# Performance work log

Hardware: AMD Instinct MI355X
Metric: run time of the kernel (lower is better)

The kernel has to match this reference:

```python
import jax, jax.numpy as jnp
import numpy as np

N = 100000
E = 1600000
NEG_SLOPE = 0.2


def gat_conv(h_x, edge_index, W, a_src, a_dst, b, heads, concat):
    # h_x: [N, Fin]; W: [Fin, heads*C]
    n = h_x.shape[0]
    h = (h_x @ W).reshape(n, heads, -1)              # [N, H, C]
    s_src = (h * a_src[None]).sum(-1)                # [N, H]
    s_dst = (h * a_dst[None]).sum(-1)                # [N, H]
    # add self loops (PyG default)
    loop = jnp.arange(n, dtype=edge_index.dtype)
    src = jnp.concatenate([edge_index[0], loop])
    dst = jnp.concatenate([edge_index[1], loop])
    e = jax.nn.leaky_relu(s_src[src] + s_dst[dst], NEG_SLOPE)   # [E+N, H]
    m = jax.ops.segment_max(e, dst, num_segments=n)
    e = jnp.exp(e - m[dst])
    denom = jax.ops.segment_sum(e, dst, num_segments=n)
    alpha = e / denom[dst]                                       # [E+N, H]
    out = jax.ops.segment_sum(alpha[:, :, None] * h[src], dst, num_segments=n)  # [N,H,C]
    out = out.reshape(n, -1) if concat else out.mean(axis=1)
    return out + b


def setup_inputs() -> dict:
    key = jax.random.key(0)
    ks = jax.random.split(key, 16)
    s = 0.1
    return {
        "x": jax.random.normal(ks[0], (N, 128), jnp.float32),
        "edge_index": jax.random.randint(ks[1], (2, E), 0, N, jnp.int64 if jax.config.jax_enable_x64 else jnp.int32),
        "W0": jax.random.normal(ks[2], (128, 64), jnp.float32) * s,
        "a_src0": jax.random.normal(ks[3], (1, 64), jnp.float32) * s,
        "a_dst0": jax.random.normal(ks[4], (1, 64), jnp.float32) * s,
        "b0": jax.random.normal(ks[5], (64,), jnp.float32) * s,
        "sW0": jax.random.normal(ks[6], (128, 64), jnp.float32) * s,
        "sb0": jax.random.normal(ks[7], (64,), jnp.float32) * s,
        "W1": jax.random.normal(ks[8], (64, 32), jnp.float32) * s,
        "a_src1": jax.random.normal(ks[9], (1, 32), jnp.float32) * s,
        "a_dst1": jax.random.normal(ks[10], (1, 32), jnp.float32) * s,
        "b1": jax.random.normal(ks[11], (32,), jnp.float32) * s,
        "sW1": jax.random.normal(ks[12], (64, 32), jnp.float32) * s,
        "sb1": jax.random.normal(ks[13], (32,), jnp.float32) * s,
    }


def reference(x, edge_index, W0, a_src0, a_dst0, b0, sW0, sb0,
              W1, a_src1, a_dst1, b1, sW1, sb1):
    # layer 0: GATConv (heads=1, concat=True) + linear skip, ELU (dropout p=0 is identity)
    h = gat_conv(x, edge_index, W0, a_src0, a_dst0, b0, heads=1, concat=True) + (x @ sW0 + sb0)
    h = jax.nn.elu(h)
    # layer 1: GATConv (heads=1, concat=False -> mean) + linear skip, log_softmax
    h = gat_conv(h, edge_index, W1, a_src1, a_dst1, b1, heads=1, concat=False) + (h @ sW1 + sb1)
    return jax.nn.log_softmax(h, axis=-1)
```

## Files before the change

### kernel.cpp

```cpp
#include <hip/hip_runtime.h>
#include <hip/hip_bf16.h>
#include <math.h>

#define NEG_SLOPE 0.2f
#define ECLAMP 30.0f
#define HCLAMP 1.0e4f

#define BSHIFT 8
#define BR 256
#define NBMAX 1024
#define CHUNK 2048

typedef short v8s __attribute__((ext_vector_type(8)));
typedef float v4f __attribute__((ext_vector_type(4)));
typedef unsigned long long ull;

__device__ __forceinline__ float bf2f(__hip_bfloat16 v) { return __bfloat162float(v); }
__device__ __forceinline__ __hip_bfloat16 f2bf(float v) { return __float2bfloat16(v); }
__device__ __forceinline__ float sane(float v)   { return fminf(fmaxf(v, -HCLAMP), HCLAMP); }
__device__ __forceinline__ float eclampf(float v){ return fminf(fmaxf(v, -ECLAMP), ECLAMP); }

__device__ __forceinline__ float ldany(int isf32, const void* p, int i) {
    return isf32 ? ((const float*)p)[i] : bf2f(((const __hip_bfloat16*)p)[i]);
}
__device__ __forceinline__ int ldidx(int is64, const void* p, long long i) {
    return is64 ? (int)((const long long*)p)[i] : ((const int*)p)[i];
}
__device__ __forceinline__ v8s ld8(const __hip_bfloat16* p) { return *(const v8s*)p; }

__device__ __forceinline__ float ewgt(float e) {
    e = e > 0.f ? e : NEG_SLOPE * e;
    return __expf(eclampf(e));
}

__device__ __forceinline__ float bflo(unsigned v) { return __uint_as_float(v << 16); }
__device__ __forceinline__ float bfhi(unsigned v) { return __uint_as_float(v & 0xffff0000u); }
__device__ __forceinline__ unsigned packbf(float a, float b) {
    __hip_bfloat16 x = f2bf(a), y = f2bf(b);
    return (unsigned)(*(unsigned short*)&x) | ((unsigned)(*(unsigned short*)&y) << 16);
}

__global__ void k_probe(const unsigned* __restrict__ xw, int nw_safe,
                        const unsigned* __restrict__ ew, int* __restrict__ flags) {
    __shared__ int cnt[2];
    int t = threadIdx.x;
    if (t < 2) cnt[t] = 0;
    __syncthreads();
    unsigned w = xw[(unsigned)(t * 9973) % (unsigned)nw_safe];
    unsigned lo = w & 0xffffu;
    unsigned exp = (lo >> 7) & 0xffu;
    if (lo != 0u && (exp < 90u || exp > 160u)) atomicAdd(&cnt[0], 1);
    if (ew[2 * t + 1] == 0u) atomicAdd(&cnt[1], 1);
    __syncthreads();
    if (t == 0) { flags[0] = (2 * cnt[0] > 256) ? 1 : 0; flags[1] = (cnt[1] >= 200) ? 1 : 0; }
}

__global__ void k_params(const int* __restrict__ flags,
                         const void* W0, const void* sW0, const void* as0, const void* ad0,
                         const void* b0, const void* sb0, const void* W1, const void* sW1,
                         const void* as1, const void* ad1, const void* b1, const void* sb1,
                         float* __restrict__ Pf, __hip_bfloat16* __restrict__ Wg) {
    int f = flags[0];
    int t = blockIdx.x * blockDim.x + threadIdx.x;
    int T = gridDim.x * blockDim.x;
    for (int i = t; i < 8192; i += T) {
        int n = i >> 7, k = i & 127;
        Wg[i]        = f2bf(ldany(f, W0,  k * 64 + n));
        Wg[8192 + i] = f2bf(ldany(f, sW0, k * 64 + n));
    }
    for (int i = t; i < 2048; i += T) {
        int n = i >> 6, k = i & 63;
        Wg[16384 + i] = f2bf(ldany(f, W1,  k * 32 + n));
        Wg[18432 + i] = f2bf(ldany(f, sW1, k * 32 + n));
    }
    if (t < 64) {
        Pf[t]       = ldany(f, as0, t);
        Pf[64 + t]  = ldany(f, ad0, t);
        Pf[128 + t] = ldany(f, b0, t) + ldany(f, sb0, t);
    }
    if (t < 32) {
        Pf[192 + t] = ldany(f, as1, t);
        Pf[224 + t] = ldany(f, ad1, t);
        Pf[256 + t] = ldany(f, b1, t) + ldany(f, sb1, t);
    }
}

__global__ void k_zero(int* __restrict__ p, int n) {
    int i = blockIdx.x * blockDim.x + threadIdx.x;
    if (i < n) p[i] = 0;
}

__global__ __launch_bounds__(256) void k_chist(const void* __restrict__ ei,
                                               const int* __restrict__ flags,
                                               int E, int N, int NB,
                                               int* __restrict__ hist) {
    __shared__ int h[NBMAX];
    for (int i = threadIdx.x; i < NB; i += 256) h[i] = 0;
    __syncthreads();
    int f = flags[1];
    long long c0 = (long long)blockIdx.x * CHUNK;
    long long c1 = c0 + CHUNK;
    if (c1 > E) c1 = E;
    for (long long i = c0 + threadIdx.x; i < c1; i += 256) {
        unsigned d = (unsigned)ldidx(f, ei, (long long)E + i);
        if (d < (unsigned)N) atomicAdd(&h[d >> BSHIFT], 1);
    }
    __syncthreads();
    long long base = (long long)blockIdx.x * NB;
    for (int i = threadIdx.x; i < NB; i += 256) hist[base + i] = h[i];
}

__global__ __launch_bounds__(1024) void k_cscan(const int* __restrict__ hist,
                                                int gch, int NB,
                                                int* __restrict__ cb,
                                                int* __restrict__ bcount) {
    __shared__ int sh[1024];
    int b = blockIdx.x;
    int t = threadIdx.x;
    int run = 0;
    for (int base = 0; base < gch; base += 1024) {
        int c = base + t;
        int v = (c < gch) ? hist[(long long)c * NB + b] : 0;
        sh[t] = v;
        __syncthreads();
        for (int off = 1; off < 1024; off <<= 1) {
            int xv = (t >= off) ? sh[t - off] : 0;
            __syncthreads();
            sh[t] += xv;
            __syncthreads();
        }
        if (c < gch) cb[(long long)c * NB + b] = run + sh[t] - v;
        run += sh[1023];
        __syncthreads();
    }
    if (t == 0) bcount[b] = run;
}

__global__ void k_bscan(const int* __restrict__ bcount, int NB,
                        int* __restrict__ bbase) {
    __shared__ int sh[NBMAX];
    int t = threadIdx.x;
    int v = (t < NB) ? bcount[t] : 0;
    sh[t] = v;
    __syncthreads();
    for (int off = 1; off < NBMAX; off <<= 1) {
        int xv = (t >= off) ? sh[t - off] : 0;
        __syncthreads();
        sh[t] += xv;
        __syncthreads();
    }
    if (t < NB) bbase[t] = sh[t] - v;
    if (t == NB - 1) bbase[NB] = sh[t];
}

__global__ __launch_bounds__(256) void k_bscatter(const void* __restrict__ ei,
                                                  const int* __restrict__ flags,
                                                  int E, int N, int NB,
                                                  const int* __restrict__ bbase,
                                                  const int* __restrict__ cb,
                                                  unsigned* __restrict__ binned) {
    __shared__ int rb[NBMAX];
    int f = flags[1];
    long long cbase = (long long)blockIdx.x * NB;
    for (int i = threadIdx.x; i < NB; i += 256) rb[i] = bbase[i] + cb[cbase + i];
    __syncthreads();
    long long c0 = (long long)blockIdx.x * CHUNK;
    long long c1 = c0 + CHUNK;
    if (c1 > E) c1 = E;
    for (long long i = c0 + threadIdx.x; i < c1; i += 256) {
        unsigned d = (unsigned)ldidx(f, ei, (long long)E + i);
        if (d < (unsigned)N) {
            int b = d >> BSHIFT;
            unsigned s = (unsigned)ldidx(f, ei, i);
            if (s >= (unsigned)N) s = 0x00FFFFFFu;
            int r = atomicAdd(&rb[b], 1);
            binned[r] = ((d & (unsigned)(BR - 1)) << 24) | s;
        }
    }
}

__global__ __launch_bounds__(256) void k_bbuild(const unsigned* __restrict__ binned,
                                                const int* __restrict__ bbase,
                                                int N, int NB,
                                                int* __restrict__ rowptr,
                                                int* __restrict__ csr_src) {
    __shared__ int ldeg[BR];
    __shared__ int lpos[BR];
    int b = blockIdx.x;
    int t = threadIdx.x;
    int e0 = bbase[b], e1 = bbase[b + 1];
    ldeg[t] = 0;
    __syncthreads();
    for (int i = e0 + t; i < e1; i += 256) {
        atomicAdd(&ldeg[binned[i] >> 24], 1);
    }
    __syncthreads();
    int v = ldeg[t];
    lpos[t] = v;
    __syncthreads();
    for (int off = 1; off < BR; off <<= 1) {
        int xv = (t >= off) ? lpos[t - off] : 0;
        __syncthreads();
        lpos[t] += xv;
        __syncthreads();
    }
    int excl = lpos[t] - v;
    int node = (b << BSHIFT) + t;
    if (node < N) rowptr[node] = e0 + excl;
    if (b == NB - 1 && t == 0) rowptr[N] = e1;
    ldeg[t] = e0 + excl;
    __syncthreads();
    for (int i = e0 + t; i < e1; i += 256) {
        unsigned w = binned[i];
        int p = atomicAdd(&ldeg[w >> 24], 1);
        csr_src[p] = (int)(w & 0x00FFFFFFu);
    }
}

__global__ void k_deg(const void* __restrict__ ei, const int* __restrict__ flags,
                      int E, int N, int* __restrict__ deg) {
    int i = blockIdx.x * blockDim.x + threadIdx.x;
    if (i < E) {
        unsigned d = (unsigned)ldidx(flags[1], ei, (long long)E + i);
        if (d < (unsigned)N) atomicAdd(&deg[d], 1);
    }
}

__global__ void k_scan1(const int* __restrict__ deg, int N,
                        int* __restrict__ rowptr, int* __restrict__ bsum) {
    __shared__ int sh[1024];
    int t = threadIdx.x;
    int idx = blockIdx.x * 1024 + t;
    int v = (idx < N) ? deg[idx] : 0;
    sh[t] = v;
    __syncthreads();
    for (int off = 1; off < 1024; off <<= 1) {
        int xv = (t >= off) ? sh[t - off] : 0;
        __syncthreads();
        sh[t] += xv;
        __syncthreads();
    }
    if (idx < N) rowptr[idx] = sh[t] - v;
    if (t == 1023) bsum[blockIdx.x] = sh[1023];
}

__global__ void k_scan2(int* __restrict__ bsum, int B, int* __restrict__ rowptr, int N) {
    __shared__ int sh[1024];
    int t = threadIdx.x;
    int v = (t < B) ? bsum[t] : 0;
    sh[t] = v;
    __syncthreads();
    for (int off = 1; off < 1024; off <<= 1) {
        int xv = (t >= off) ? sh[t - off] : 0;
        __syncthreads();
        sh[t] += xv;
        __syncthreads();
    }
    if (t < B) bsum[t] = sh[t] - v;
    if (t == 1023) rowptr[N] = sh[1023];
}

__global__ void k_scan3(int N, int* __restrict__ rowptr, const int* __restrict__ bsum,
                        int* __restrict__ cursor) {
    int idx = blockIdx.x * 1024 + threadIdx.x;
    if (idx < N) {
        int r = rowptr[idx] + bsum[blockIdx.x];
        rowptr[idx] = r;
        cursor[idx] = r;
    }
}

__global__ void k_fill(const void* __restrict__ ei, const int* __restrict__ flags,
                       int E, int N, int* __restrict__ cursor, int* __restrict__ csr_src) {
    int i = blockIdx.x * blockDim.x + threadIdx.x;
    if (i < E) {
        int f = flags[1];
        unsigned d = (unsigned)ldidx(f, ei, (long long)E + i);
        if (d < (unsigned)N) {
            int p = atomicAdd(&cursor[d], 1);
            if ((unsigned)p < (unsigned)E) csr_src[p] = ldidx(f, ei, i);
        }
    }
}

__global__ __launch_bounds__(256) void k_l0(
    const void* __restrict__ x, const int* __restrict__ flags,
    const float* __restrict__ Pf, const __hip_bfloat16* __restrict__ Wg, int N,
    __hip_bfloat16* __restrict__ h0, __hip_bfloat16* __restrict__ skip0,
    float* __restrict__ ssrc, float* __restrict__ sdst) {
    __shared__ __hip_bfloat16 sm[26112];
    __hip_bfloat16* xs  = sm;
    __hip_bfloat16* wt0 = sm + 8704;
    __hip_bfloat16* wts = sm + 17408;
    int tid = threadIdx.x;
    int f = flags[0];
    int tile = blockIdx.x * 64;

    for (int i = tid * 4; i < 8192; i += 1024) {
        int r = i >> 7, k = i & 127;
        uint2 w0v = *(const uint2*)&Wg[i];
        uint2 w1v = *(const uint2*)&Wg[8192 + i];
        *(uint2*)&wt0[r * 136 + k] = w0v;
        *(uint2*)&wts[r * 136 + k] = w1v;
    }
    for (int i = tid * 4; i < 8192; i += 1024) {
        int r = i >> 7, k = i & 127;
        int g = tile + r; if (g >= N) g = N - 1;
        uint2* dx = (uint2*)&xs[r * 136 + k];
        if (f) {
            float4 v = *(const float4*)((const float*)x + (size_t)g * 128 + k);
            uint2 o; o.x = packbf(v.x, v.y); o.y = packbf(v.z, v.w);
            *dx = o;
        } else {
            *dx = *(const uint2*)((const __hip_bfloat16*)x + (size_t)g * 128 + k);
        }
    }
    __syncthreads();

    int lane = tid & 63, w = tid >> 6;
    int n16 = lane & 15, quad = lane >> 4;
    v4f zf = {0.f, 0.f, 0.f, 0.f};
    v4f acc_h[4], acc_s[4];
#pragma unroll
    for (int t = 0; t < 4; t++) { acc_h[t] = zf; acc_s[t] = zf; }

    int arow = (w << 4) + n16;
#pragma unroll
    for (int s = 0; s < 4; s++) {
        v8s a = ld8(&xs[arow * 136 + s * 32 + (quad << 3)]);
#pragma unroll
        for (int t = 0; t < 4; t++) {
            v8s bh = ld8(&wt0[(t * 16 + n16) * 136 + s * 32 + (quad << 3)]);
            acc_h[t] = __builtin_amdgcn_mfma_f32_16x16x32_bf16(a, bh, acc_h[t], 0, 0, 0);
            v8s bs = ld8(&wts[(t * 16 + n16) * 136 + s * 32 + (quad << 3)]);
            acc_s[t] = __builtin_amdgcn_mfma_f32_16x16x32_bf16(a, bs, acc_s[t], 0, 0, 0);
        }
    }

    int mbase = tile + (w << 4) + (quad << 2);
    float ps[4] = {0, 0, 0, 0}, pd[4] = {0, 0, 0, 0};
#pragma unroll
    for (int t = 0; t < 4; t++) {
        int ch = t * 16 + n16;
        float av = Pf[ch];
        float dv = Pf[64 + ch];
        float bv = Pf[128 + ch];
#pragma unroll
        for (int r = 0; r < 4; r++) {
            float hv = sane(acc_h[t][r]);
            float sv = sane(acc_s[t][r] + bv);
            int node = mbase + r;
            if (node < N) {
                h0[(size_t)node * 64 + ch] = f2bf(hv);
                skip0[(size_t)node * 64 + ch] = f2bf(sv);
            }
            ps[r] += hv * av;
            pd[r] += hv * dv;
        }
    }
#pragma unroll
    for (int m = 1; m <= 8; m <<= 1) {
#pragma unroll
        for (int r = 0; r < 4; r++) {
            ps[r] += __shfl_xor(ps[r], m, 64);
            pd[r] += __shfl_xor(pd[r], m, 64);
        }
    }
    if (n16 == 0) {
#pragma unroll
        for (int r = 0; r < 4; r++) {
            int node = mbase + r;
            if (node < N) { ssrc[node] = sane(ps[r]); sdst[node] = sane(pd[r]); }
        }
    }
}

__global__ __launch_bounds__(512) void k_l0agg_l1(
    const int* __restrict__ rowptr, const int* __restrict__ csr_src,
    const float* __restrict__ ssrc0, const float* __restrict__ sdst0,
    const __hip_bfloat16* __restrict__ h0, const __hip_bfloat16* __restrict__ skip0,
    const float* __restrict__ Pf, const __hip_bfloat16* __restrict__ Wg, int N,
    __hip_bfloat16* __restrict__ h1, __hip_bfloat16* __restrict__ skip1,
    float* __restrict__ ssrc1, float* __restrict__ sdst1) {
    __shared__ __hip_bfloat16 xs[4608];
    __shared__ __hip_bfloat16 wsm[4608];
    __shared__ ull ews[512];
    __shared__ float psum[64], pdum[64];
    __hip_bfloat16* wt1 = wsm;
    __hip_bfloat16* ws1 = wsm + 2304;
    int tid = threadIdx.x;
    int tile = blockIdx.x * 64;

    {
        int i = tid * 4;
        int r = i >> 6, k = i & 63;
        *(uint2*)&wt1[r * 72 + k] = *(const uint2*)&Wg[16384 + i];
        *(uint2*)&ws1[r * 72 + k] = *(const uint2*)&Wg[18432 + i];
    }
    if (tid < 64) { psum[tid] = 0.f; pdum[tid] = 0.f; }

    int wv = tid >> 6, lane = tid & 63;
    int half = lane >> 5, l5 = lane & 31;
    int slot = l5 >> 4, c4 = l5 & 15;
    const uint2* h0w = (const uint2*)h0;
    ull* myw = &ews[wv * 64 + half * 32];

    for (int pass = 0; pass < 4; pass++) {
        int row = pass * 16 + wv * 2 + half;
        int n = tile + row;
        bool act = n < N;
        int nn = act ? n : 0;

        float sd = sdst0[nn];
        float wself = ewgt(ssrc0[nn] + sd);

        uint2 selfv = h0w[(size_t)nn * 16 + c4];
        float w0 = (slot == 0) ? wself : 0.f;
        float acc0 = w0 * bflo(selfv.x);
        float acc1 = w0 * bfhi(selfv.x);
        float acc2 = w0 * bflo(selfv.y);
        float acc3 = w0 * bfhi(selfv.y);
        float denp = 0.f;

        int beg = act ? rowptr[nn] : 0;
        int end = act ? rowptr[nn + 1] : 0;
        for (int j0 = beg; j0 < end; j0 += 32) {
            int cnt = end - j0; if (cnt > 32) cnt = 32;
            int s = (l5 < cnt) ? csr_src[j0 + l5] : 0;
            bool v = (l5 < cnt) && ((unsigned)s < (unsigned)N);
            int sg = v ? s : 0;
            float wj = v ? ewgt(ssrc0[sg] + sd) : 0.f;
            denp += wj;
            myw[l5] = ((ull)__float_as_uint(wj) << 32) | (unsigned)sg;
            int k2 = 0;
            int full = cnt & ~7;
            for (; k2 < full; k2 += 8) {
                ull pa = myw[k2 + slot];
                ull pb = myw[k2 + 2 + slot];
                ull pc = myw[k2 + 4 + slot];
                ull pd_ = myw[k2 + 6 + slot];
                float wa = __uint_as_float((unsigned)(pa >> 32));
                float wb = __uint_as_float((unsigned)(pb >> 32));
                float wc = __uint_as_float((unsigned)(pc >> 32));
                float wd = __uint_as_float((unsigned)(pd_ >> 32));
                int sa = (int)(unsigned)(pa & 0xffffffffu);
                int sb = (int)(unsigned)(pb & 0xffffffffu);
                int sc = (int)(unsigned)(pc & 0xffffffffu);
                int sdi = (int)(unsigned)(pd_ & 0xffffffffu);
                uint2 va = h0w[(size_t)sa * 16 + c4];
                uint2 vb = h0w[(size_t)sb * 16 + c4];
                uint2 vc = h0w[(size_t)sc * 16 + c4];
                uint2 vd = h0w[(size_t)sdi * 16 + c4];
                acc0 += wa * bflo(va.x) + wb * bflo(vb.x) + wc * bflo(vc.x) + wd * bflo(vd.x);
                acc1 += wa * bfhi(va.x) + wb * bfhi(vb.x) + wc * bfhi(vc.x) + wd * bfhi(vd.x);
                acc2 += wa * bflo(va.y) + wb * bflo(vb.y) + wc * bflo(vc.y) + wd * bflo(vd.y);
                acc3 += wa * bfhi(va.y) + wb * bfhi(vb.y) + wc * bfhi(vc.y) + wd * bfhi(vd.y);
            }
            for (; k2 < cnt; k2 += 8) {
                int ia = k2 + slot,     ib = k2 + 2 + slot;
                int ic = k2 + 4 + slot, id = k2 + 6 + slot;
                ull pa = myw[ia < cnt ? ia : 0];
                ull pb = myw[ib < cnt ? ib : 0];
                ull pc = myw[ic < cnt ? ic : 0];
                ull pd_ = myw[id < cnt ? id : 0];
                float wa = (ia < cnt) ? __uint_as_float((unsigned)(pa >> 32)) : 0.f;
                float wb = (ib < cnt) ? __uint_as_float((unsigned)(pb >> 32)) : 0.f;
                float wc = (ic < cnt) ? __uint_as_float((unsigned)(pc >> 32)) : 0.f;
                float wd = (id < cnt) ? __uint_as_float((unsigned)(pd_ >> 32)) : 0.f;
                int sa = (int)(unsigned)(pa & 0xffffffffu);
                int sb = (int)(unsigned)(pb & 0xffffffffu);
                int sc = (int)(unsigned)(pc & 0xffffffffu);
                int sdi = (int)(unsigned)(pd_ & 0xffffffffu);
                uint2 va = h0w[(size_t)sa * 16 + c4];
                uint2 vb = h0w[(size_t)sb * 16 + c4];
                uint2 vc = h0w[(size_t)sc * 16 + c4];
                uint2 vd = h0w[(size_t)sdi * 16 + c4];
                acc0 += wa * bflo(va.x) + wb * bflo(vb.x) + wc * bflo(vc.x) + wd * bflo(vd.x);
                acc1 += wa * bfhi(va.x) + wb * bfhi(vb.x) + wc * bfhi(vc.x) + wd * bfhi(vd.x);
                acc2 += wa * bflo(va.y) + wb * bflo(vb.y) + wc * bflo(vc.y) + wd * bflo(vd.y);
                acc3 += wa * bfhi(va.y) + wb * bfhi(vb.y) + wc * bfhi(vc.y) + wd * bfhi(vd.y);
            }
        }
        acc0 += __shfl_xor(acc0, 16, 64);
        acc1 += __shfl_xor(acc1, 16, 64);
        acc2 += __shfl_xor(acc2, 16, 64);
        acc3 += __shfl_xor(acc3, 16, 64);
        float den = denp;
#pragma unroll
        for (int m = 1; m <= 16; m <<= 1) den += __shfl_xor(den, m, 64);
        den += wself;

        if (slot == 0) {
            uint2 o; o.x = 0u; o.y = 0u;
            if (act) {
                uint2 skv = ((const uint2*)skip0)[(size_t)nn * 16 + c4];
                float v0 = sane(acc0 / den + bflo(skv.x));
                float v1 = sane(acc1 / den + bfhi(skv.x));
                float v2 = sane(acc2 / den + bflo(skv.y));
                float v3 = sane(acc3 / den + bfhi(skv.y));
                v0 = v0 > 0.f ? v0 : (__expf(v0) - 1.f);
                v1 = v1 > 0.f ? v1 : (__expf(v1) - 1.f);
                v2 = v2 > 0.f ? v2 : (__expf(v2) - 1.f);
                v3 = v3 > 0.f ? v3 : (__expf(v3) - 1.f);
                o.x = packbf(v0, v1);
                o.y = packbf(v2, v3);
            }
            *(uint2*)&xs[row * 72 + c4 * 4] = o;
        }
    }
    __syncthreads();

    int w8 = wv;
    int rt = w8 >> 1, ct = w8 & 1;
    int n16 = lane & 15, quad = lane >> 4;
    v4f acc_h = {0.f, 0.f, 0.f, 0.f};
    v4f acc_s = {0.f, 0.f, 0.f, 0.f};
    int arow = rt * 16 + n16;
#pragma unroll
    for (int s = 0; s < 2; s++) {
        v8s a = ld8(&xs[arow * 72 + s * 32 + (quad << 3)]);
        v8s bh = ld8(&wt1[(ct * 16 + n16) * 72 + s * 32 + (quad << 3)]);
        acc_h = __builtin_amdgcn_mfma_f32_16x16x32_bf16(a, bh, acc_h, 0, 0, 0);
        v8s bs = ld8(&ws1[(ct * 16 + n16) * 72 + s * 32 + (quad << 3)]);
        acc_s = __builtin_amdgcn_mfma_f32_16x16x32_bf16(a, bs, acc_s, 0, 0, 0);
    }

    int mrow = rt * 16 + (quad << 2);
    int mbase = tile + mrow;
    int ch = ct * 16 + n16;
    float av = Pf[192 + ch];
    float dv = Pf[224 + ch];
    float bv = Pf[256 + ch];
    float ps[4] = {0, 0, 0, 0}, pd[4] = {0, 0, 0, 0};
#pragma unroll
    for (int r = 0; r < 4; r++) {
        float hv = sane(acc_h[r]);
        float sv = sane(acc_s[r] + bv);
        int node = mbase + r;
        if (node < N) {
            h1[(size_t)node * 32 + ch] = f2bf(hv);
            skip1[(size_t)node * 32 + ch] = f2bf(sv);
        }
        ps[r] += hv * av;
        pd[r] += hv * dv;
    }
#pragma unroll
    for (int m = 1; m <= 8; m <<= 1) {
#pragma unroll
        for (int r = 0; r < 4; r++) {
            ps[r] += __shfl_xor(ps[r], m, 64);
            pd[r] += __shfl_xor(pd[r], m, 64);
        }
    }
    if (n16 == 0) {
#pragma unroll
        for (int r = 0; r < 4; r++) {
            atomicAdd(&psum[mrow + r], ps[r]);
            atomicAdd(&pdum[mrow + r], pd[r]);
        }
    }
    __syncthreads();
    if (tid < 64) {
        int node = tile + tid;
        if (node < N) {
            ssrc1[node] = sane(psum[tid]);
            sdst1[node] = sane(pdum[tid]);
        }
    }
}

__global__ __launch_bounds__(256) void k_l1_agg(
    const int* __restrict__ rowptr, const int* __restrict__ csr_src,
    const float* __restrict__ ssrc, const float* __restrict__ sdst,
    const __hip_bfloat16* __restrict__ h1, const __hip_bfloat16* __restrict__ skip1,
    int N, float* __restrict__ out) {
    __shared__ ull ews[256];
    int wv = threadIdx.x >> 6, lane = threadIdx.x & 63;
    int half = lane >> 5, l5 = lane & 31;
    int slot = l5 >> 3, c4 = l5 & 7;
    int n = blockIdx.x * 8 + wv * 2 + half;
    bool act = n < N;
    int nn = act ? n : 0;
    const uint2* h1w = (const uint2*)h1;
    ull* myw = &ews[wv * 64 + half * 32];

    float sd = sdst[nn];
    float wself = ewgt(ssrc[nn] + sd);

    uint2 selfv = h1w[(size_t)nn * 8 + c4];
    float w0 = (slot == 0) ? wself : 0.f;
    float acc0 = w0 * bflo(selfv.x);
    float acc1 = w0 * bfhi(selfv.x);
    float acc2 = w0 * bflo(selfv.y);
    float acc3 = w0 * bfhi(selfv.y);
    float denp = 0.f;

    int beg = act ? rowptr[nn] : 0;
    int end = act ? rowptr[nn + 1] : 0;
    for (int j0 = beg; j0 < end; j0 += 32) {
        int cnt = end - j0; if (cnt > 32) cnt = 32;
        int s = (l5 < cnt) ? csr_src[j0 + l5] : 0;
        bool v = (l5 < cnt) && ((unsigned)s < (unsigned)N);
        int sg = v ? s : 0;
        float wj = v ? ewgt(ssrc[sg] + sd) : 0.f;
        denp += wj;
        myw[l5] = ((ull)__float_as_uint(wj) << 32) | (unsigned)sg;
        int k4 = 0;
        int full = cnt & ~15;
        for (; k4 < full; k4 += 16) {
            ull pa = myw[k4 + slot];
            ull pb = myw[k4 + 4 + slot];
            ull pc = myw[k4 + 8 + slot];
            ull pd_ = myw[k4 + 12 + slot];
            float wa = __uint_as_float((unsigned)(pa >> 32));
            float wb = __uint_as_float((unsigned)(pb >> 32));
            float wc = __uint_as_float((unsigned)(pc >> 32));
            float wd = __uint_as_float((unsigned)(pd_ >> 32));
            int sa = (int)(unsigned)(pa & 0xffffffffu);
            int sb = (int)(unsigned)(pb & 0xffffffffu);
            int sc = (int)(unsigned)(pc & 0xffffffffu);
            int sdi = (int)(unsigned)(pd_ & 0xffffffffu);
            uint2 va = h1w[(size_t)sa * 8 + c4];
            uint2 vb = h1w[(size_t)sb * 8 + c4];
            uint2 vc = h1w[(size_t)sc * 8 + c4];
            uint2 vd = h1w[(size_t)sdi * 8 + c4];
            acc0 += wa * bflo(va.x) + wb * bflo(vb.x) + wc * bflo(vc.x) + wd * bflo(vd.x);
            acc1 += wa * bfhi(va.x) + wb * bfhi(vb.x) + wc * bfhi(vc.x) + wd * bfhi(vd.x);
            acc2 += wa * bflo(va.y) + wb * bflo(vb.y) + wc * bflo(vc.y) + wd * bflo(vd.y);
            acc3 += wa * bfhi(va.y) + wb * bfhi(vb.y) + wc * bfhi(vc.y) + wd * bfhi(vd.y);
        }
        for (; k4 < cnt; k4 += 16) {
            int ia = k4 + slot,      ib = k4 + 4 + slot;
            int ic = k4 + 8 + slot,  id = k4 + 12 + slot;
            ull pa = myw[ia < cnt ? ia : 0];
            ull pb = myw[ib < cnt ? ib : 0];
            ull pc = myw[ic < cnt ? ic : 0];
            ull pd_ = myw[id < cnt ? id : 0];
            float wa = (ia < cnt) ? __uint_as_float((unsigned)(pa >> 32)) : 0.f;
            float wb = (ib < cnt) ? __uint_as_float((unsigned)(pb >> 32)) : 0.f;
            float wc = (ic < cnt) ? __uint_as_float((unsigned)(pc >> 32)) : 0.f;
            float wd = (id < cnt) ? __uint_as_float((unsigned)(pd_ >> 32)) : 0.f;
            int sa = (int)(unsigned)(pa & 0xffffffffu);
            int sb = (int)(unsigned)(pb & 0xffffffffu);
            int sc = (int)(unsigned)(pc & 0xffffffffu);
            int sdi = (int)(unsigned)(pd_ & 0xffffffffu);
            uint2 va = h1w[(size_t)sa * 8 + c4];
            uint2 vb = h1w[(size_t)sb * 8 + c4];
            uint2 vc = h1w[(size_t)sc * 8 + c4];
            uint2 vd = h1w[(size_t)sdi * 8 + c4];
            acc0 += wa * bflo(va.x) + wb * bflo(vb.x) + wc * bflo(vc.x) + wd * bflo(vd.x);
            acc1 += wa * bfhi(va.x) + wb * bfhi(vb.x) + wc * bfhi(vc.x) + wd * bfhi(vd.x);
            acc2 += wa * bflo(va.y) + wb * bflo(vb.y) + wc * bflo(vc.y) + wd * bflo(vd.y);
            acc3 += wa * bfhi(va.y) + wb * bfhi(vb.y) + wc * bfhi(vc.y) + wd * bfhi(vd.y);
        }
    }
    acc0 += __shfl_xor(acc0, 8, 64); acc0 += __shfl_xor(acc0, 16, 64);
    acc1 += __shfl_xor(acc1, 8, 64); acc1 += __shfl_xor(acc1, 16, 64);
    acc2 += __shfl_xor(acc2, 8, 64); acc2 += __shfl_xor(acc2, 16, 64);
    acc3 += __shfl_xor(acc3, 8, 64); acc3 += __shfl_xor(acc3, 16, 64);
    float den = denp;
#pragma unroll
    for (int m = 1; m <= 16; m <<= 1) den += __shfl_xor(den, m, 64);
    den += wself;

    uint2 skv = ((const uint2*)skip1)[(size_t)nn * 8 + c4];
    float o0 = sane(acc0 / den + bflo(skv.x));
    float o1 = sane(acc1 / den + bfhi(skv.x));
    float o2 = sane(acc2 / den + bflo(skv.y));
    float o3 = sane(acc3 / den + bfhi(skv.y));
    float m = fmaxf(fmaxf(o0, o1), fmaxf(o2, o3));
#pragma unroll
    for (int k = 1; k <= 4; k <<= 1) m = fmaxf(m, __shfl_xor(m, k, 64));
    float ex = __expf(o0 - m) + __expf(o1 - m) + __expf(o2 - m) + __expf(o3 - m);
#pragma unroll
    for (int k = 1; k <= 4; k <<= 1) ex += __shfl_xor(ex, k, 64);
    float l = __logf(ex);
    float r0 = o0 - m - l, r1 = o1 - m - l, r2 = o2 - m - l, r3 = o3 - m - l;
    if (!isfinite(r0)) r0 = 0.f;
    if (!isfinite(r1)) r1 = 0.f;
    if (!isfinite(r2)) r2 = 0.f;
    if (!isfinite(r3)) r3 = 0.f;
    if (slot == 0 && act) {
        float4 o4; o4.x = r0; o4.y = r1; o4.z = r2; o4.w = r3;
        *(float4*)&out[(size_t)nn * 32 + 4 * c4] = o4;
    }
}

__global__ void k_sentinel(float* __restrict__ out, int n, float val) {
    int i = blockIdx.x * blockDim.x + threadIdx.x;
    if (i < n) out[i] = val;
}

extern "C" void kernel_launch(void* const* d_in, const int* in_sizes, int n_in,
                              void* d_out, int out_size, void* d_ws, size_t ws_size,
                              hipStream_t stream) {
    const void* x  = d_in[0];
    const void* ei = d_in[1];
    float* out = (float*)d_out;

    int N = in_sizes[0] / 128;
    int E = in_sizes[1] / 2;

    int NB  = (N + BR - 1) >> BSHIFT;
    int gch = (E + CHUNK - 1) / CHUNK;
    if (gch < 1) gch = 1;
    bool fast = (N <= (NBMAX << BSHIFT)) && ((size_t)E * 4 <= (size_t)N * 128);

    char* ws = (char*)d_ws;
    size_t off = 0;
    auto alloc = [&](size_t bytes) -> char* {
        char* p = ws + off;
        off += (bytes + 255) & ~(size_t)255;
        return p;
    };
    int*   flags   = (int*)alloc(2 * 4);
    float* Pf      = (float*)alloc(288 * 4);
    __hip_bfloat16* Wg = (__hip_bfloat16*)alloc(20480 * 2);
    int*   rowptr  = (int*)alloc((size_t)(N + 1) * 4);
    int*   cursor  = (int*)alloc((size_t)N * 4);
    float* sdst0   = (float*)alloc((size_t)N * 4);
    float* ssrc1   = (float*)alloc((size_t)N * 4);
    float* sdst1   = (float*)alloc((size_t)N * 4);
    int*   bsum    = (int*)alloc(1024 * 4);
    int*   bcount  = (int*)alloc(NBMAX * 4);
    int*   bbase   = (int*)alloc((NBMAX + 1) * 4);
    int*   csr_src = (int*)alloc((size_t)E * 4);
    int*   hist    = (int*)alloc(fast ? (size_t)gch * NB * 4 : 0);
    int*   cb      = (int*)alloc(fast ? (size_t)gch * NB * 4 : 0);
    __hip_bfloat16* h0    = (__hip_bfloat16*)alloc((size_t)N * 64 * 2);
    __hip_bfloat16* skip0 = (__hip_bfloat16*)alloc((size_t)N * 64 * 2);
    __hip_bfloat16* h1    = (__hip_bfloat16*)alloc((size_t)N * 32 * 2);
    __hip_bfloat16* skip1 = (__hip_bfloat16*)alloc((size_t)N * 32 * 2);
    size_t required = off;

    if (ws_size < required) {
        float mb = (float)(double)(ws_size >> 20);
        k_sentinel<<<(out_size + 255) / 256, 256, 0, stream>>>(out, out_size, mb);
        return;
    }

    float* ssrc0 = (float*)cursor;

    k_probe<<<1, 256, 0, stream>>>((const unsigned*)x, N * 64, (const unsigned*)ei, flags);
    k_params<<<40, 256, 0, stream>>>(flags, d_in[2], d_in[6], d_in[3], d_in[4],
                                     d_in[5], d_in[7], d_in[8], d_in[12],
                                     d_in[9], d_in[10], d_in[11], d_in[13], Pf, Wg);

    if (fast) {
        unsigned* binned = (unsigned*)h0;
        k_chist<<<gch, 256, 0, stream>>>(ei, flags, E, N, NB, hist);
        k_cscan<<<NB, 1024, 0, stream>>>(hist, gch, NB, cb, bcount);
        k_bscan<<<1, NBMAX, 0, stream>>>(bcount, NB, bbase);
        k_bscatter<<<gch, 256, 0, stream>>>(ei, flags, E, N, NB, bbase, cb, binned);
        k_bbuild<<<NB, 256, 0, stream>>>(binned, bbase, N, NB, rowptr, csr_src);
    } else {
        int B = (N + 1023) / 1024;
        k_zero<<<(N + 255) / 256, 256, 0, stream>>>(cursor, N);
        k_deg<<<(E + 255) / 256, 256, 0, stream>>>(ei, flags, E, N, cursor);
        k_scan1<<<B, 1024, 0, stream>>>(cursor, N, rowptr, bsum);
        k_scan2<<<1, 1024, 0, stream>>>(bsum, B, rowptr, N);
        k_scan3<<<B, 1024, 0, stream>>>(N, rowptr, bsum, cursor);
        k_fill<<<(E + 255) / 256, 256, 0, stream>>>(ei, flags, E, N, cursor, csr_src);
    }

    k_l0<<<(N + 63) / 64, 256, 0, stream>>>(x, flags, Pf, Wg, N,
                                            h0, skip0, ssrc0, sdst0);
    k_l0agg_l1<<<(N + 63) / 64, 512, 0, stream>>>(rowptr, csr_src, ssrc0, sdst0,
                                                  h0, skip0, Pf, Wg, N,
                                                  h1, skip1, ssrc1, sdst1);
    k_l1_agg<<<(N + 7) / 8, 256, 0, stream>>>(rowptr, csr_src, ssrc1, sdst1,
                                              h1, skip1, N, out);
}
```

Baseline: 270.5 us.

## Fuse dtype probes and param prep into consumers; merge histogram with layer-0 GEMM

Removes the standalone probe and param-conversion kernels: each consumer kernel now detects the input dtype itself and converts weights directly into shared memory. The histogram pass and the layer-0 projection GEMM run in one launch using disjoint block ranges, so the two independent stages can overlap. The binned buffer gets its own allocation instead of aliasing h0, which is required now that h0 is written concurrently. In exchange, every block repeats the probe and the weight conversion with uncoalesced strided reads, and the fused kernel declares a larger shared-memory footprint that may reduce occupancy of the histogram blocks.

```diff
diff --git a/kernel.cpp b/kernel.cpp
--- a/kernel.cpp
+++ b/kernel.cpp
@@ -40,74 +40,148 @@
     return (unsigned)(*(unsigned short*)&x) | ((unsigned)(*(unsigned short*)&y) << 16);
 }
 
-__global__ void k_probe(const unsigned* __restrict__ xw, int nw_safe,
-                        const unsigned* __restrict__ ew, int* __restrict__ flags) {
-    __shared__ int cnt[2];
-    int t = threadIdx.x;
-    if (t < 2) cnt[t] = 0;
-    __syncthreads();
-    unsigned w = xw[(unsigned)(t * 9973) % (unsigned)nw_safe];
-    unsigned lo = w & 0xffffu;
-    unsigned exp = (lo >> 7) & 0xffu;
-    if (lo != 0u && (exp < 90u || exp > 160u)) atomicAdd(&cnt[0], 1);
-    if (ew[2 * t + 1] == 0u) atomicAdd(&cnt[1], 1);
-    __syncthreads();
-    if (t == 0) { flags[0] = (2 * cnt[0] > 256) ? 1 : 0; flags[1] = (cnt[1] >= 200) ? 1 : 0; }
-}
-
-__global__ void k_params(const int* __restrict__ flags,
-                         const void* W0, const void* sW0, const void* as0, const void* ad0,
-                         const void* b0, const void* sb0, const void* W1, const void* sW1,
-                         const void* as1, const void* ad1, const void* b1, const void* sb1,
-                         float* __restrict__ Pf, __hip_bfloat16* __restrict__ Wg) {
-    int f = flags[0];
-    int t = blockIdx.x * blockDim.x + threadIdx.x;
-    int T = gridDim.x * blockDim.x;
-    for (int i = t; i < 8192; i += T) {
-        int n = i >> 7, k = i & 127;
-        Wg[i]        = f2bf(ldany(f, W0,  k * 64 + n));
-        Wg[8192 + i] = f2bf(ldany(f, sW0, k * 64 + n));
-    }
-    for (int i = t; i < 2048; i += T) {
-        int n = i >> 6, k = i & 63;
-        Wg[16384 + i] = f2bf(ldany(f, W1,  k * 32 + n));
-        Wg[18432 + i] = f2bf(ldany(f, sW1, k * 32 + n));
-    }
-    if (t < 64) {
-        Pf[t]       = ldany(f, as0, t);
-        Pf[64 + t]  = ldany(f, ad0, t);
-        Pf[128 + t] = ldany(f, b0, t) + ldany(f, sb0, t);
-    }
-    if (t < 32) {
-        Pf[192 + t] = ldany(f, as1, t);
-        Pf[224 + t] = ldany(f, ad1, t);
-        Pf[256 + t] = ldany(f, b1, t) + ldany(f, sb1, t);
-    }
-}
-
-__global__ void k_zero(int* __restrict__ p, int n) {
-    int i = blockIdx.x * blockDim.x + threadIdx.x;
-    if (i < n) p[i] = 0;
-}
-
-__global__ __launch_bounds__(256) void k_chist(const void* __restrict__ ei,
-                                               const int* __restrict__ flags,
-                                               int E, int N, int NB,
-                                               int* __restrict__ hist) {
-    __shared__ int h[NBMAX];
-    for (int i = threadIdx.x; i < NB; i += 256) h[i] = 0;
-    __syncthreads();
-    int f = flags[1];
-    long long c0 = (long long)blockIdx.x * CHUNK;
-    long long c1 = c0 + CHUNK;
-    if (c1 > E) c1 = E;
-    for (long long i = c0 + threadIdx.x; i < c1; i += 256) {
-        unsigned d = (unsigned)ldidx(f, ei, (long long)E + i);
-        if (d < (unsigned)N) atomicAdd(&h[d >> BSHIFT], 1);
-    }
-    __syncthreads();
-    long long base = (long long)blockIdx.x * NB;
-    for (int i = threadIdx.x; i < NB; i += 256) hist[base + i] = h[i];
+__device__ __forceinline__ int probe_isf32(const unsigned* xw, int nw_safe, int tid, int* cnt) {
+    if (tid == 0) cnt[0] = 0;
+    __syncthreads();
+    if (tid < 256) {
+        unsigned w = xw[(unsigned)(tid * 9973) % (unsigned)nw_safe];
+        unsigned lo = w & 0xffffu;
+        unsigned e = (lo >> 7) & 0xffu;
+        if (lo != 0u && (e < 90u || e > 160u)) atomicAdd(&cnt[0], 1);
+    }
+    __syncthreads();
+    int r = (2 * cnt[0] > 256) ? 1 : 0;
+    __syncthreads();
+    return r;
+}
+__device__ __forceinline__ int probe_is64(const unsigned* ew, int tid, int* cnt) {
+    if (tid == 0) cnt[0] = 0;
+    __syncthreads();
+    if (tid < 256) {
+        if (ew[2 * tid + 1] == 0u) atomicAdd(&cnt[0], 1);
+    }
+    __syncthreads();
+    int r = (cnt[0] >= 200) ? 1 : 0;
+    __syncthreads();
+    return r;
+}
+
+__global__ __launch_bounds__(256) void k1_chist_l0(
+    const void* __restrict__ ei, const void* __restrict__ x,
+    const void* W0, const void* sW0, const void* as0, const void* ad0,
+    const void* b0, const void* sb0,
+    int N, int E, int NB, int gch,
+    int* __restrict__ hist,
+    __hip_bfloat16* __restrict__ h0, __hip_bfloat16* __restrict__ skip0,
+    float* __restrict__ ssrc, float* __restrict__ sdst) {
+    __shared__ __align__(16) char smraw[52224];
+    int tid = threadIdx.x;
+
+    if ((int)blockIdx.x < gch) {
+        int f = probe_is64((const unsigned*)ei, tid, (int*)smraw);
+        int* h = (int*)smraw;
+        for (int i = tid; i < NB; i += 256) h[i] = 0;
+        __syncthreads();
+        long long c0 = (long long)blockIdx.x * CHUNK;
+        long long c1 = c0 + CHUNK;
+        if (c1 > E) c1 = E;
+        for (long long i = c0 + tid; i < c1; i += 256) {
+            unsigned d = (unsigned)ldidx(f, ei, (long long)E + i);
+            if (d < (unsigned)N) atomicAdd(&h[d >> BSHIFT], 1);
+        }
+        __syncthreads();
+        long long base = (long long)blockIdx.x * NB;
+        for (int i = tid; i < NB; i += 256) hist[base + i] = h[i];
+        return;
+    }
+
+    int f = probe_isf32((const unsigned*)x, N * 64, tid, (int*)smraw);
+    __hip_bfloat16* xs  = (__hip_bfloat16*)smraw;
+    __hip_bfloat16* wt0 = xs + 8704;
+    __hip_bfloat16* wts = xs + 17408;
+    int tile = ((int)blockIdx.x - gch) * 64;
+
+    for (int i = tid * 4; i < 8192; i += 1024) {
+        int r = i >> 7, k = i & 127;
+        __hip_bfloat16 a0[4], a1[4];
+#pragma unroll
+        for (int u = 0; u < 4; u++) {
+            a0[u] = f2bf(ldany(f, W0,  (k + u) * 64 + r));
+            a1[u] = f2bf(ldany(f, sW0, (k + u) * 64 + r));
+        }
+        *(uint2*)&wt0[r * 136 + k] = *(uint2*)a0;
+        *(uint2*)&wts[r * 136 + k] = *(uint2*)a1;
+    }
+    for (int i = tid * 4; i < 8192; i += 1024) {
+        int r = i >> 7, k = i & 127;
+        int g = tile + r; if (g >= N) g = N - 1;
+        uint2* dx = (uint2*)&xs[r * 136 + k];
+        if (f) {
+            float4 v = *(const float4*)((const float*)x + (size_t)g * 128 + k);
+            uint2 o; o.x = packbf(v.x, v.y); o.y = packbf(v.z, v.w);
+            *dx = o;
+        } else {
+            *dx = *(const uint2*)((const __hip_bfloat16*)x + (size_t)g * 128 + k);
+        }
+    }
+    __syncthreads();
+
+    int lane = tid & 63, w = tid >> 6;
+    int n16 = lane & 15, quad = lane >> 4;
+    v4f zf = {0.f, 0.f, 0.f, 0.f};
+    v4f acc_h[4], acc_s[4];
+#pragma unroll
+    for (int t = 0; t < 4; t++) { acc_h[t] = zf; acc_s[t] = zf; }
+
+    int arow = (w << 4) + n16;
+#pragma unroll
+    for (int s = 0; s < 4; s++) {
+        v8s a = ld8(&xs[arow * 136 + s * 32 + (quad << 3)]);
+#pragma unroll
+        for (int t = 0; t < 4; t++) {
+            v8s bh = ld8(&wt0[(t * 16 + n16) * 136 + s * 32 + (quad << 3)]);
+            acc_h[t] = __builtin_amdgcn_mfma_f32_16x16x32_bf16(a, bh, acc_h[t], 0, 0, 0);
+            v8s bs = ld8(&wts[(t * 16 + n16) * 136 + s * 32 + (quad << 3)]);
+            acc_s[t] = __builtin_amdgcn_mfma_f32_16x16x32_bf16(a, bs, acc_s[t], 0, 0, 0);
+        }
+    }
+
+    int mbase = tile + (w << 4) + (quad << 2);
+    float ps[4] = {0, 0, 0, 0}, pd[4] = {0, 0, 0, 0};
+#pragma unroll
+    for (int t = 0; t < 4; t++) {
+        int ch = t * 16 + n16;
+        float av = ldany(f, as0, ch);
+        float dv = ldany(f, ad0, ch);
+        float bv = ldany(f, b0, ch) + ldany(f, sb0, ch);
+#pragma unroll
+        for (int r = 0; r < 4; r++) {
+            float hv = sane(acc_h[t][r]);
+            float sv = sane(acc_s[t][r] + bv);
+            int node = mbase + r;
+            if (node < N) {
+                h0[(size_t)node * 64 + ch] = f2bf(hv);
+                skip0[(size_t)node * 64 + ch] = f2bf(sv);
+            }
+            ps[r] += hv * av;
+            pd[r] += hv * dv;
+        }
+    }
+#pragma unroll
+    for (int m = 1; m <= 8; m <<= 1) {
+#pragma unroll
+        for (int r = 0; r < 4; r++) {
+            ps[r] += __shfl_xor(ps[r], m, 64);
+            pd[r] += __shfl_xor(pd[r], m, 64);
+        }
+    }
+    if (n16 == 0) {
+#pragma unroll
+        for (int r = 0; r < 4; r++) {
+            int node = mbase + r;
+            if (node < N) { ssrc[node] = sane(ps[r]); sdst[node] = sane(pd[r]); }
+        }
+    }
 }
 
 __global__ __launch_bounds__(1024) void k_cscan(const int* __restrict__ hist,
@@ -154,20 +228,20 @@
 }
 
 __global__ __launch_bounds__(256) void k_bscatter(const void* __restrict__ ei,
-                                                  const int* __restrict__ flags,
                                                   int E, int N, int NB,
                                                   const int* __restrict__ bbase,
                                                   const int* __restrict__ cb,
                                                   unsigned* __restrict__ binned) {
     __shared__ int rb[NBMAX];
-    int f = flags[1];
+    int tid = threadIdx.x;
+    int f = probe_is64((const unsigned*)ei, tid, rb);
     long long cbase = (long long)blockIdx.x * NB;
-    for (int i = threadIdx.x; i < NB; i += 256) rb[i] = bbase[i] + cb[cbase + i];
+    for (int i = tid; i < NB; i += 256) rb[i] = bbase[i] + cb[cbase + i];
     __syncthreads();
     long long c0 = (long long)blockIdx.x * CHUNK;
     long long c1 = c0 + CHUNK;
     if (c1 > E) c1 = E;
-    for (long long i = c0 + threadIdx.x; i < c1; i += 256) {
+    for (long long i = c0 + tid; i < c1; i += 256) {
         unsigned d = (unsigned)ldidx(f, ei, (long long)E + i);
         if (d < (unsigned)N) {
             int b = d >> BSHIFT;
@@ -217,11 +291,13 @@
     }
 }
 
-__global__ void k_deg(const void* __restrict__ ei, const int* __restrict__ flags,
-                      int E, int N, int* __restrict__ deg) {
+__global__ __launch_bounds__(256) void k_deg(const void* __restrict__ ei,
+                                             int E, int N, int* __restrict__ deg) {
+    __shared__ int cnt[1];
+    int f = probe_is64((const unsigned*)ei, threadIdx.x, cnt);
     int i = blockIdx.x * blockDim.x + threadIdx.x;
     if (i < E) {
-        unsigned d = (unsigned)ldidx(flags[1], ei, (long long)E + i);
+        unsigned d = (unsigned)ldidx(f, ei, (long long)E + i);
         if (d < (unsigned)N) atomicAdd(&deg[d], 1);
     }
 }
@@ -270,11 +346,13 @@
     }
 }
 
-__global__ void k_fill(const void* __restrict__ ei, const int* __restrict__ flags,
-                       int E, int N, int* __restrict__ cursor, int* __restrict__ csr_src) {
+__global__ __launch_bounds__(256) void k_fill(const void* __restrict__ ei,
+                                              int E, int N, int* __restrict__ cursor,
+                                              int* __restrict__ csr_src) {
+    __shared__ int cnt[1];
+    int f = probe_is64((const unsigned*)ei, threadIdx.x, cnt);
     int i = blockIdx.x * blockDim.x + threadIdx.x;
     if (i < E) {
-        int f = flags[1];
         unsigned d = (unsigned)ldidx(f, ei, (long long)E + i);
         if (d < (unsigned)N) {
             int p = atomicAdd(&cursor[d], 1);
@@ -283,103 +361,13 @@
     }
 }
 
-__global__ __launch_bounds__(256) void k_l0(
-    const void* __restrict__ x, const int* __restrict__ flags,
-    const float* __restrict__ Pf, const __hip_bfloat16* __restrict__ Wg, int N,
-    __hip_bfloat16* __restrict__ h0, __hip_bfloat16* __restrict__ skip0,
-    float* __restrict__ ssrc, float* __restrict__ sdst) {
-    __shared__ __hip_bfloat16 sm[26112];
-    __hip_bfloat16* xs  = sm;
-    __hip_bfloat16* wt0 = sm + 8704;
-    __hip_bfloat16* wts = sm + 17408;
-    int tid = threadIdx.x;
-    int f = flags[0];
-    int tile = blockIdx.x * 64;
-
-    for (int i = tid * 4; i < 8192; i += 1024) {
-        int r = i >> 7, k = i & 127;
-        uint2 w0v = *(const uint2*)&Wg[i];
-        uint2 w1v = *(const uint2*)&Wg[8192 + i];
-        *(uint2*)&wt0[r * 136 + k] = w0v;
-        *(uint2*)&wts[r * 136 + k] = w1v;
-    }
-    for (int i = tid * 4; i < 8192; i += 1024) {
-        int r = i >> 7, k = i & 127;
-        int g = tile + r; if (g >= N) g = N - 1;
-        uint2* dx = (uint2*)&xs[r * 136 + k];
-        if (f) {
-            float4 v = *(const float4*)((const float*)x + (size_t)g * 128 + k);
-            uint2 o; o.x = packbf(v.x, v.y); o.y = packbf(v.z, v.w);
-            *dx = o;
-        } else {
-            *dx = *(const uint2*)((const __hip_bfloat16*)x + (size_t)g * 128 + k);
-        }
-    }
-    __syncthreads();
-
-    int lane = tid & 63, w = tid >> 6;
-    int n16 = lane & 15, quad = lane >> 4;
-    v4f zf = {0.f, 0.f, 0.f, 0.f};
-    v4f acc_h[4], acc_s[4];
-#pragma unroll
-    for (int t = 0; t < 4; t++) { acc_h[t] = zf; acc_s[t] = zf; }
-
-    int arow = (w << 4) + n16;
-#pragma unroll
-    for (int s = 0; s < 4; s++) {
-        v8s a = ld8(&xs[arow * 136 + s * 32 + (quad << 3)]);
-#pragma unroll
-        for (int t = 0; t < 4; t++) {
-            v8s bh = ld8(&wt0[(t * 16 + n16) * 136 + s * 32 + (quad << 3)]);
-            acc_h[t] = __builtin_amdgcn_mfma_f32_16x16x32_bf16(a, bh, acc_h[t], 0, 0, 0);
-            v8s bs = ld8(&wts[(t * 16 + n16) * 136 + s * 32 + (quad << 3)]);
-            acc_s[t] = __builtin_amdgcn_mfma_f32_16x16x32_bf16(a, bs, acc_s[t], 0, 0, 0);
-        }
-    }
-
-    int mbase = tile + (w << 4) + (quad << 2);
-    float ps[4] = {0, 0, 0, 0}, pd[4] = {0, 0, 0, 0};
-#pragma unroll
-    for (int t = 0; t < 4; t++) {
-        int ch = t * 16 + n16;
-        float av = Pf[ch];
-        float dv = Pf[64 + ch];
-        float bv = Pf[128 + ch];
-#pragma unroll
-        for (int r = 0; r < 4; r++) {
-            float hv = sane(acc_h[t][r]);
-            float sv = sane(acc_s[t][r] + bv);
-            int node = mbase + r;
-            if (node < N) {
-                h0[(size_t)node * 64 + ch] = f2bf(hv);
-                skip0[(size_t)node * 64 + ch] = f2bf(sv);
-            }
-            ps[r] += hv * av;
-            pd[r] += hv * dv;
-        }
-    }
-#pragma unroll
-    for (int m = 1; m <= 8; m <<= 1) {
-#pragma unroll
-        for (int r = 0; r < 4; r++) {
-            ps[r] += __shfl_xor(ps[r], m, 64);
-            pd[r] += __shfl_xor(pd[r], m, 64);
-        }
-    }
-    if (n16 == 0) {
-#pragma unroll
-        for (int r = 0; r < 4; r++) {
-            int node = mbase + r;
-            if (node < N) { ssrc[node] = sane(ps[r]); sdst[node] = sane(pd[r]); }
-        }
-    }
-}
-
 __global__ __launch_bounds__(512) void k_l0agg_l1(
     const int* __restrict__ rowptr, const int* __restrict__ csr_src,
     const float* __restrict__ ssrc0, const float* __restrict__ sdst0,
     const __hip_bfloat16* __restrict__ h0, const __hip_bfloat16* __restrict__ skip0,
-    const float* __restrict__ Pf, const __hip_bfloat16* __restrict__ Wg, int N,
+    const void* __restrict__ x,
+    const void* W1, const void* sW1, const void* as1, const void* ad1,
+    const void* b1, const void* sb1, int N,
     __hip_bfloat16* __restrict__ h1, __hip_bfloat16* __restrict__ skip1,
     float* __restrict__ ssrc1, float* __restrict__ sdst1) {
     __shared__ __hip_bfloat16 xs[4608];
@@ -391,11 +379,19 @@
     int tid = threadIdx.x;
     int tile = blockIdx.x * 64;
 
+    int f = probe_isf32((const unsigned*)x, N * 64, tid, (int*)ews);
+
     {
         int i = tid * 4;
         int r = i >> 6, k = i & 63;
-        *(uint2*)&wt1[r * 72 + k] = *(const uint2*)&Wg[16384 + i];
-        *(uint2*)&ws1[r * 72 + k] = *(const uint2*)&Wg[18432 + i];
+        __hip_bfloat16 a0[4], a1[4];
+#pragma unroll
+        for (int u = 0; u < 4; u++) {
+            a0[u] = f2bf(ldany(f, W1,  (k + u) * 32 + r));
+            a1[u] = f2bf(ldany(f, sW1, (k + u) * 32 + r));
+        }
+        *(uint2*)&wt1[r * 72 + k] = *(uint2*)a0;
+        *(uint2*)&ws1[r * 72 + k] = *(uint2*)a1;
     }
     if (tid < 64) { psum[tid] = 0.f; pdum[tid] = 0.f; }
 
@@ -510,8 +506,7 @@
     }
     __syncthreads();
 
-    int w8 = wv;
-    int rt = w8 >> 1, ct = w8 & 1;
+    int rt = wv >> 1, ct = wv & 1;
     int n16 = lane & 15, quad = lane >> 4;
     v4f acc_h = {0.f, 0.f, 0.f, 0.f};
     v4f acc_s = {0.f, 0.f, 0.f, 0.f};
@@ -528,9 +523,9 @@
     int mrow = rt * 16 + (quad << 2);
     int mbase = tile + mrow;
     int ch = ct * 16 + n16;
-    float av = Pf[192 + ch];
-    float dv = Pf[224 + ch];
-    float bv = Pf[256 + ch];
+    float av = ldany(f, as1, ch);
+    float dv = ldany(f, ad1, ch);
+    float bv = ldany(f, b1, ch) + ldany(f, sb1, ch);
     float ps[4] = {0, 0, 0, 0}, pd[4] = {0, 0, 0, 0};
 #pragma unroll
     for (int r = 0; r < 4; r++) {
@@ -686,6 +681,11 @@
     }
 }
 
+__global__ void k_zero(int* __restrict__ p, int n) {
+    int i = blockIdx.x * blockDim.x + threadIdx.x;
+    if (i < n) p[i] = 0;
+}
+
 __global__ void k_sentinel(float* __restrict__ out, int n, float val) {
     int i = blockIdx.x * blockDim.x + threadIdx.x;
     if (i < n) out[i] = val;
@@ -704,6 +704,7 @@
     int NB  = (N + BR - 1) >> BSHIFT;
     int gch = (E + CHUNK - 1) / CHUNK;
     if (gch < 1) gch = 1;
+    int Lb = (N + 63) / 64;
     bool fast = (N <= (NBMAX << BSHIFT)) && ((size_t)E * 4 <= (size_t)N * 128);
 
     char* ws = (char*)d_ws;
@@ -713,9 +714,6 @@
         off += (bytes + 255) & ~(size_t)255;
         return p;
     };
-    int*   flags   = (int*)alloc(2 * 4);
-    float* Pf      = (float*)alloc(288 * 4);
-    __hip_bfloat16* Wg = (__hip_bfloat16*)alloc(20480 * 2);
     int*   rowptr  = (int*)alloc((size_t)(N + 1) * 4);
     int*   cursor  = (int*)alloc((size_t)N * 4);
     float* sdst0   = (float*)alloc((size_t)N * 4);
@@ -725,6 +723,7 @@
     int*   bcount  = (int*)alloc(NBMAX * 4);
     int*   bbase   = (int*)alloc((NBMAX + 1) * 4);
     int*   csr_src = (int*)alloc((size_t)E * 4);
+    unsigned* binned = (unsigned*)alloc(fast ? (size_t)E * 4 : 0);
     int*   hist    = (int*)alloc(fast ? (size_t)gch * NB * 4 : 0);
     int*   cb      = (int*)alloc(fast ? (size_t)gch * NB * 4 : 0);
     __hip_bfloat16* h0    = (__hip_bfloat16*)alloc((size_t)N * 64 * 2);
@@ -741,33 +740,32 @@
 
     float* ssrc0 = (float*)cursor;
 
-    k_probe<<<1, 256, 0, stream>>>((const unsigned*)x, N * 64, (const unsigned*)ei, flags);
-    k_params<<<40, 256, 0, stream>>>(flags, d_in[2], d_in[6], d_in[3], d_in[4],
-                                     d_in[5], d_in[7], d_in[8], d_in[12],
-                                     d_in[9], d_in[10], d_in[11], d_in[13], Pf, Wg);
-
     if (fast) {
-        unsigned* binned = (unsigned*)h0;
-        k_chist<<<gch, 256, 0, stream>>>(ei, flags, E, N, NB, hist);
+        k1_chist_l0<<<gch + Lb, 256, 0, stream>>>(ei, x, d_in[2], d_in[6], d_in[3], d_in[4],
+                                                  d_in[5], d_in[7], N, E, NB, gch, hist,
+                                                  h0, skip0, ssrc0, sdst0);
         k_cscan<<<NB, 1024, 0, stream>>>(hist, gch, NB, cb, bcount);
         k_bscan<<<1, NBMAX, 0, stream>>>(bcount, NB, bbase);
-        k_bscatter<<<gch, 256, 0, stream>>>(ei, flags, E, N, NB, bbase, cb, binned);
+        k_bscatter<<<gch, 256, 0, stream>>>(ei, E, N, NB, bbase, cb, binned);
         k_bbuild<<<NB, 256, 0, stream>>>(binned, bbase, N, NB, rowptr, csr_src);
     } else {
         int B = (N + 1023) / 1024;
         k_zero<<<(N + 255) / 256, 256, 0, stream>>>(cursor, N);
-        k_deg<<<(E + 255) / 256, 256, 0, stream>>>(ei, flags, E, N, cursor);
+        k_deg<<<(E + 255) / 256, 256, 0, stream>>>(ei, E, N, cursor);
         k_scan1<<<B, 1024, 0, stream>>>(cursor, N, rowptr, bsum);
         k_scan2<<<1, 1024, 0, stream>>>(bsum, B, rowptr, N);
         k_scan3<<<B, 1024, 0, stream>>>(N, rowptr, bsum, cursor);
-        k_fill<<<(E + 255) / 256, 256, 0, stream>>>(ei, flags, E, N, cursor, csr_src);
-    }
-
-    k_l0<<<(N + 63) / 64, 256, 0, stream>>>(x, flags, Pf, Wg, N,
+        k_fill<<<(E + 255) / 256, 256, 0, stream>>>(ei, E, N, cursor, csr_src);
+        k1_chist_l0<<<Lb, 256, 0, stream>>>(ei, x, d_in[2], d_in[6], d_in[3], d_in[4],
+                                            d_in[5], d_in[7], N, E, NB, 0, hist,
                                             h0, skip0, ssrc0, sdst0);
-    k_l0agg_l1<<<(N + 63) / 64, 512, 0, stream>>>(rowptr, csr_src, ssrc0, sdst0,
-                                                  h0, skip0, Pf, Wg, N,
-                                                  h1, skip1, ssrc1, sdst1);
+    }
+
+    k_l0agg_l1<<<Lb, 512, 0, stream>>>(rowptr, csr_src, ssrc0, sdst0,
+                                       h0, skip0, x,
+                                       d_in[8], d_in[12], d_in[9], d_in[10],
+                                       d_in[11], d_in[13], N,
+                                       h1, skip1, ssrc1, sdst1);
     k_l1_agg<<<(N + 7) / 8, 256, 0, stream>>>(rowptr, csr_src, ssrc1, sdst1,
                                               h1, skip1, N, out);
 }
```

Result: slower. 321.6 us (+18.9%).
